# Optimization experiments

Hardware: AMD Instinct MI355X
Metric: run time of the kernel (lower is better)

The kernel has to match this reference:

```python
import jax, jax.numpy as jnp
import numpy as np

N_ATOM = 10000
D = 256
N_EDGE = 160000
BN_EPS = 1e-6


def _bn_eval(x, g, b, m, v):
    # BatchNorm1d in eval mode
    return (x - m) * jax.lax.rsqrt(v + BN_EPS) * g + b


def setup_inputs() -> dict:
    key = jax.random.key(0)
    ks = jax.random.split(key, 12)
    def glorot(k, shape):
        fan_in = shape[-1]
        return jax.random.normal(k, shape, dtype=jnp.float32) / np.sqrt(fan_in)
    inp = {
        'atom': jax.random.normal(ks[0], (N_ATOM, D), dtype=jnp.float32),
        'bond_index': jax.random.randint(ks[1], (2, N_EDGE), 0, N_ATOM, dtype=jnp.int32),
        # align: Linear(2D -> 1) + BN(1)
        'W_align': glorot(ks[2], (1, 2 * D)),
        'b_align': jnp.zeros((1,), jnp.float32),
        'bn_a_g': jnp.ones((1,), jnp.float32),
        'bn_a_b': jnp.zeros((1,), jnp.float32),
        'bn_a_m': jnp.zeros((1,), jnp.float32),
        'bn_a_v': jnp.ones((1,), jnp.float32),
        # attend: Linear(D -> D) + BN(D)
        'W_att': glorot(ks[3], (D, D)),
        'b_att': jnp.zeros((D,), jnp.float32),
        'bn_t_g': jnp.ones((D,), jnp.float32),
        'bn_t_b': jnp.zeros((D,), jnp.float32),
        'bn_t_m': jnp.zeros((D,), jnp.float32),
        'bn_t_v': jnp.ones((D,), jnp.float32),
        # GRUCell(D, D): weights stacked [r; z; n] as in torch
        'W_ih': glorot(ks[4], (3 * D, D)),
        'W_hh': glorot(ks[5], (3 * D, D)),
        'b_ih': jnp.zeros((3 * D,), jnp.float32),
        'b_hh': jnp.zeros((3 * D,), jnp.float32),
    }
    return inp


def reference(atom, bond_index, W_align, b_align, bn_a_g, bn_a_b, bn_a_m, bn_a_v,
              W_att, b_att, bn_t_g, bn_t_b, bn_t_m, bn_t_v,
              W_ih, W_hh, b_ih, b_hh):
    num_atom = atom.shape[0]
    src = bond_index[0]
    dst = bond_index[1]

    # gather + concat: [E, 2D]
    feat_align = jnp.concatenate([atom[src], atom[dst]], axis=-1)
    # align score: Linear(2D->1) + BN + leaky_relu -> [E, 1]
    s = feat_align @ W_align.T + b_align
    s = _bn_eval(s, bn_a_g, bn_a_b, bn_a_m, bn_a_v)
    s = jax.nn.leaky_relu(s, negative_slope=0.01)

    # segment softmax over edges grouped by src atom
    seg_max = jax.ops.segment_max(s, src, num_segments=num_atom)  # [N, 1]
    e = jnp.exp(s - seg_max[src])
    denom = jax.ops.segment_sum(e, src, num_segments=num_atom)    # [N, 1]
    attn = e / (denom[src] + 1e-8)                                # [E, 1]

    # attend: Linear(D->D) + BN on gathered dst features
    h = atom[dst] @ W_att.T + b_att
    h = _bn_eval(h, bn_t_g, bn_t_b, bn_t_m, bn_t_v)

    # weighted scatter-add aggregation -> [N, D], then ELU
    context = jax.ops.segment_sum(attn * h, src, num_segments=num_atom)
    context = jax.nn.elu(context)

    # GRUCell: input=context, hidden=atom
    gi = context @ W_ih.T + b_ih   # [N, 3D]
    gh = atom @ W_hh.T + b_hh      # [N, 3D]
    i_r, i_z, i_n = jnp.split(gi, 3, axis=-1)
    h_r, h_z, h_n = jnp.split(gh, 3, axis=-1)
    r = jax.nn.sigmoid(i_r + h_r)
    z = jax.nn.sigmoid(i_z + h_z)
    n = jnp.tanh(i_n + r * h_n)
    update = (1.0 - z) * n + z * atom
    return update
```

## Files before the change

kernel.cpp:

```cpp
#include <hip/hip_runtime.h>
#include <hip/hip_bf16.h>

#define D 256

typedef __attribute__((ext_vector_type(8))) short bf16x8;
typedef __attribute__((ext_vector_type(4))) short s16x4;
typedef __attribute__((ext_vector_type(4))) float f32x4;

#define MFMA __builtin_amdgcn_mfma_f32_16x16x32_bf16

__device__ __forceinline__ float s2f(short u) {
    union { unsigned int i; float f; } c;
    c.i = ((unsigned int)(unsigned short)u) << 16;
    return c.f;
}
__device__ __forceinline__ short f2s(float f) {
    union { float f; unsigned int u; } c; c.f = f;
    unsigned int u = c.u;
    u += 0x7fffu + ((u >> 16) & 1u);
    return (short)(u >> 16);
}

__global__ __launch_bounds__(256) void prep_kernel(
    const float* __restrict__ atom, short* __restrict__ atom_bf,
    const float* __restrict__ W_align, const float* __restrict__ b_align,
    const float* __restrict__ g, const float* __restrict__ bb,
    const float* __restrict__ mn, const float* __restrict__ vr,
    float* __restrict__ p0p, float* __restrict__ p1p,
    const float* __restrict__ Wa, short* __restrict__ Wa_bf,
    const float* __restrict__ Wi, short* __restrict__ Wi_bf,
    const float* __restrict__ Wh, short* __restrict__ Wh_bf,
    int* __restrict__ cnt, int* __restrict__ cursor,
    int N, int NROWB, int WCVTB)
{
    int b = blockIdx.x, tid = threadIdx.x;
    if (b < NROWB) {
        int wave = tid >> 6, lane = tid & 63;
        int row = b * 4 + wave;
        if (row >= N) return;
        float4 a = *(const float4*)(atom + (size_t)row * D + lane * 4);
        s16x4 o; o[0] = f2s(a.x); o[1] = f2s(a.y); o[2] = f2s(a.z); o[3] = f2s(a.w);
        ((s16x4*)(atom_bf + (size_t)row * D))[lane] = o;
        float4 w0 = *(const float4*)(W_align + lane * 4);
        float4 w1 = *(const float4*)(W_align + D + lane * 4);
        float d0 = a.x * w0.x + a.y * w0.y + a.z * w0.z + a.w * w0.w;
        float d1 = a.x * w1.x + a.y * w1.y + a.z * w1.z + a.w * w1.w;
        #pragma unroll
        for (int s = 32; s > 0; s >>= 1) {
            d0 += __shfl_xor(d0, s, 64);
            d1 += __shfl_xor(d1, s, 64);
        }
        if (lane == 0) {
            float A = rsqrtf(vr[0] + 1e-6f) * g[0];
            p0p[row] = A * (d0 + b_align[0]) + bb[0] - A * mn[0];
            p1p[row] = A * d1;
        }
        return;
    }
    b -= NROWB;
    if (b < WCVTB) {
        int nW4 = D * D / 4, nG4 = 3 * D * D / 4;
        int j = b * 256 + tid;
        const float* src; short* dst;
        if (j < nW4) { src = Wa; dst = Wa_bf; }
        else { j -= nW4;
            if (j < nG4) { src = Wi; dst = Wi_bf; }
            else { j -= nG4;
                if (j < nG4) { src = Wh; dst = Wh_bf; }
                else return;
            }
        }
        float4 v = ((const float4*)src)[j];
        s16x4 o; o[0] = f2s(v.x); o[1] = f2s(v.y); o[2] = f2s(v.z); o[3] = f2s(v.w);
        ((s16x4*)dst)[j] = o;
        return;
    }
    b -= WCVTB;
    int i = b * 256 + tid;
    if (i < N) { cnt[i] = 0; cursor[i] = 0; }
}

__global__ __launch_bounds__(256) void count_kernel(const int* __restrict__ src, int* cnt, int E) {
    int e = blockIdx.x * 256 + threadIdx.x;
    if (e < E) atomicAdd(&cnt[src[e]], 1);
}

__global__ __launch_bounds__(1024) void scan_kernel(const int* __restrict__ cnt, int* __restrict__ off, int N) {
    __shared__ int sums[1024];
    int t = threadIdx.x;
    int CH = (N + 1023) / 1024;
    int beg = t * CH;
    int end = beg + CH; if (end > N) end = N;
    int s = 0;
    for (int i = beg; i < end; i++) s += cnt[i];
    sums[t] = s;
    __syncthreads();
    for (int d = 1; d < 1024; d <<= 1) {
        int x = (t >= d) ? sums[t - d] : 0;
        __syncthreads();
        sums[t] += x;
        __syncthreads();
    }
    int run = (t > 0) ? sums[t - 1] : 0;
    for (int i = beg; i < end; i++) { off[i] = run; run += cnt[i]; }
    if (end == N) off[N] = run;
}

__global__ __launch_bounds__(256) void fill_kernel(const int* __restrict__ src, const int* __restrict__ dst,
                                                   const int* __restrict__ off, int* cursor, int* dlist, int E) {
    int e = blockIdx.x * 256 + threadIdx.x;
    if (e < E) {
        int s = src[e];
        int p = atomicAdd(&cursor[s], 1);
        dlist[off[s] + p] = dst[e];
    }
}

__global__ __launch_bounds__(256) void hA_kernel(
    const short* __restrict__ atom_bf, const short* __restrict__ W_bf,
    const float* __restrict__ bias,
    const float* __restrict__ g, const float* __restrict__ bb,
    const float* __restrict__ mn, const float* __restrict__ vr,
    short* __restrict__ hA, int N, int NB)
{
    __shared__ short Bs[2048 * 8];
    int bi = blockIdx.x;
    int xcd = bi & 7, rest = bi >> 3;
    int cb = rest & 3, gh = rest >> 2;
    int gg = gh * 8 + xcd;
    if (gg >= NB) return;
    int c0 = cb * 64;
    int tid = threadIdx.x;
    for (int c = tid; c < 2048; c += 256) {
        int l15c = c & 15, quadc = (c >> 4) & 3, t2 = c >> 6;
        int kkc = t2 & 7, jc = t2 >> 3;
        bf16x8 v = *(const bf16x8*)(W_bf + (size_t)(c0 + jc * 16 + l15c) * D + quadc * 8 + kkc * 32);
        *(bf16x8*)(&Bs[c * 8]) = v;
    }
    __syncthreads();

    int wave = tid >> 6, lane = tid & 63;
    int quad = lane >> 4, l15 = lane & 15;
    int m0 = gg * 128 + wave * 16;
    int ar0 = m0 + l15;       if (ar0 > N - 1) ar0 = N - 1;
    int ar1 = m0 + 64 + l15;  if (ar1 > N - 1) ar1 = N - 1;
    const short* ap0 = atom_bf + (size_t)ar0 * D + quad * 8;
    const short* ap1 = atom_bf + (size_t)ar1 * D + quad * 8;
    const short* lb = &Bs[lane * 8];
    f32x4 acc[2][4];
    #pragma unroll
    for (int t = 0; t < 2; t++)
        #pragma unroll
        for (int j = 0; j < 4; j++) acc[t][j] = (f32x4){0,0,0,0};
    #pragma unroll
    for (int kk = 0; kk < 8; kk++) {
        int k = kk * 32;
        bf16x8 a0 = *(const bf16x8*)(ap0 + k);
        bf16x8 a1 = *(const bf16x8*)(ap1 + k);
        bf16x8 b0 = *(const bf16x8*)(lb + (0 * 8 + kk) * 512);
        bf16x8 b1 = *(const bf16x8*)(lb + (1 * 8 + kk) * 512);
        bf16x8 b2 = *(const bf16x8*)(lb + (2 * 8 + kk) * 512);
        bf16x8 b3 = *(const bf16x8*)(lb + (3 * 8 + kk) * 512);
        acc[0][0] = MFMA(a0, b0, acc[0][0], 0, 0, 0);
        acc[0][1] = MFMA(a0, b1, acc[0][1], 0, 0, 0);
        acc[0][2] = MFMA(a0, b2, acc[0][2], 0, 0, 0);
        acc[0][3] = MFMA(a0, b3, acc[0][3], 0, 0, 0);
        acc[1][0] = MFMA(a1, b0, acc[1][0], 0, 0, 0);
        acc[1][1] = MFMA(a1, b1, acc[1][1], 0, 0, 0);
        acc[1][2] = MFMA(a1, b2, acc[1][2], 0, 0, 0);
        acc[1][3] = MFMA(a1, b3, acc[1][3], 0, 0, 0);
    }
    #pragma unroll
    for (int j = 0; j < 4; j++) {
        int col = c0 + j * 16 + l15;
        float sc = rsqrtf(vr[col] + 1e-6f) * g[col];
        float sh = bb[col] - mn[col] * sc;
        float bi_ = bias[col];
        #pragma unroll
        for (int t = 0; t < 2; t++) {
            #pragma unroll
            for (int r = 0; r < 4; r++) {
                int row = m0 + t * 64 + quad * 4 + r;
                if (row < N) hA[(size_t)row * D + col] = f2s((acc[t][j][r] + bi_) * sc + sh);
            }
        }
    }
}

__global__ __launch_bounds__(256) void agg_kernel(
    const int* __restrict__ off, const int* __restrict__ dlist,
    const float* __restrict__ p0p, const float* __restrict__ p1p,
    const short* __restrict__ hA, short* __restrict__ ctx, int N)
{
    int w = (blockIdx.x * blockDim.x + threadIdx.x) >> 6;
    int lane = threadIdx.x & 63;
    if (w >= N) return;
    int beg = off[w], end = off[w + 1];
    float u = p0p[w];
    int half = lane >> 5, l32 = lane & 31;
    float acc[8] = {0.f,0.f,0.f,0.f,0.f,0.f,0.f,0.f};
    float se = 0.f;
    for (int j = beg + half; j < end; j += 2) {
        int d = dlist[j];
        float x = u + p1p[d];
        x = x > 0.f ? x : 0.01f * x;
        float e = __expf(x);
        se += e;
        bf16x8 h = *(const bf16x8*)(hA + (size_t)d * D + l32 * 8);
        #pragma unroll
        for (int i = 0; i < 8; i++) acc[i] += e * s2f(h[i]);
    }
    se += __shfl_xor(se, 32, 64);
    #pragma unroll
    for (int i = 0; i < 8; i++) acc[i] += __shfl_xor(acc[i], 32, 64);
    if (half == 0) {
        float inv = 1.f / (se + 1e-8f);
        bf16x8 o;
        #pragma unroll
        for (int i = 0; i < 8; i++) {
            float v = acc[i] * inv;
            v = v > 0.f ? v : __expf(v) - 1.f;
            o[i] = f2s(v);
        }
        *(bf16x8*)(ctx + (size_t)w * D + l32 * 8) = o;
    }
}

__global__ __launch_bounds__(256) void gru_kernel(
    const short* __restrict__ ctx, const short* __restrict__ atom_bf,
    const short* __restrict__ W_ih, const short* __restrict__ W_hh,
    const float* __restrict__ b_ih, const float* __restrict__ b_hh,
    float* __restrict__ out, int N, int NB)
{
    __shared__ short Bs[3072 * 8];
    int bi = blockIdx.x;
    int xcd = bi & 7, rest = bi >> 3;
    int cb = rest & 15, gh = rest >> 4;
    int gg = gh * 8 + xcd;
    if (gg >= NB) return;
    int c0 = cb * 16;
    int tid = threadIdx.x;
    for (int c = tid; c < 3072; c += 256) {
        int l15c = c & 15, quadc = (c >> 4) & 3, t2 = c >> 6;
        int kkc = t2 & 7, gate = t2 >> 3;
        const short* srcp = (gate < 3)
            ? W_ih + (size_t)(gate * 256 + c0 + l15c) * D + quadc * 8 + kkc * 32
            : W_hh + (size_t)((gate - 3) * 256 + c0 + l15c) * D + quadc * 8 + kkc * 32;
        *(bf16x8*)(&Bs[c * 8]) = *(const bf16x8*)srcp;
    }
    __syncthreads();

    int wave = tid >> 6, lane = tid & 63;
    int quad = lane >> 4, l15 = lane & 15;
    int m0 = gg * 128 + wave * 16;
    int ar0 = m0 + l15;       if (ar0 > N - 1) ar0 = N - 1;
    int ar1 = m0 + 64 + l15;  if (ar1 > N - 1) ar1 = N - 1;
    const short* cp0 = ctx + (size_t)ar0 * D + quad * 8;
    const short* ap0 = atom_bf + (size_t)ar0 * D + quad * 8;
    const short* cp1 = ctx + (size_t)ar1 * D + quad * 8;
    const short* ap1 = atom_bf + (size_t)ar1 * D + quad * 8;
    const short* lb = &Bs[lane * 8];
    f32x4 gi[2][3], gh_[2][3];
    #pragma unroll
    for (int t = 0; t < 2; t++)
        #pragma unroll
        for (int j = 0; j < 3; j++) { gi[t][j] = (f32x4){0,0,0,0}; gh_[t][j] = (f32x4){0,0,0,0}; }
    #pragma unroll
    for (int kk = 0; kk < 8; kk++) {
        int k = kk * 32;
        bf16x8 c0v = *(const bf16x8*)(cp0 + k);
        bf16x8 a0v = *(const bf16x8*)(ap0 + k);
        bf16x8 c1v = *(const bf16x8*)(cp1 + k);
        bf16x8 a1v = *(const bf16x8*)(ap1 + k);
        bf16x8 bir = *(const bf16x8*)(lb + (0 * 8 + kk) * 512);
        bf16x8 biz = *(const bf16x8*)(lb + (1 * 8 + kk) * 512);
        bf16x8 bin = *(const bf16x8*)(lb + (2 * 8 + kk) * 512);
        bf16x8 bhr = *(const bf16x8*)(lb + (3 * 8 + kk) * 512);
        bf16x8 bhz = *(const bf16x8*)(lb + (4 * 8 + kk) * 512);
        bf16x8 bhn = *(const bf16x8*)(lb + (5 * 8 + kk) * 512);
        gi[0][0] = MFMA(c0v, bir, gi[0][0], 0, 0, 0);
        gi[0][1] = MFMA(c0v, biz, gi[0][1], 0, 0, 0);
        gi[0][2] = MFMA(c0v, bin, gi[0][2], 0, 0, 0);
        gh_[0][0] = MFMA(a0v, bhr, gh_[0][0], 0, 0, 0);
        gh_[0][1] = MFMA(a0v, bhz, gh_[0][1], 0, 0, 0);
        gh_[0][2] = MFMA(a0v, bhn, gh_[0][2], 0, 0, 0);
        gi[1][0] = MFMA(c1v, bir, gi[1][0], 0, 0, 0);
        gi[1][1] = MFMA(c1v, biz, gi[1][1], 0, 0, 0);
        gi[1][2] = MFMA(c1v, bin, gi[1][2], 0, 0, 0);
        gh_[1][0] = MFMA(a1v, bhr, gh_[1][0], 0, 0, 0);
        gh_[1][1] = MFMA(a1v, bhz, gh_[1][1], 0, 0, 0);
        gh_[1][2] = MFMA(a1v, bhn, gh_[1][2], 0, 0, 0);
    }
    int col = c0 + l15;
    float bir_s = b_ih[col], biz_s = b_ih[col + 256], bin_s = b_ih[col + 512];
    float bhr_s = b_hh[col], bhz_s = b_hh[col + 256], bhn_s = b_hh[col + 512];
    #pragma unroll
    for (int t = 0; t < 2; t++) {
        #pragma unroll
        for (int r = 0; r < 4; r++) {
            int row = m0 + t * 64 + quad * 4 + r;
            if (row < N) {
                float rr = 1.f / (1.f + __expf(-(gi[t][0][r] + bir_s + gh_[t][0][r] + bhr_s)));
                float zz = 1.f / (1.f + __expf(-(gi[t][1][r] + biz_s + gh_[t][1][r] + bhz_s)));
                float nn = tanhf(gi[t][2][r] + bin_s + rr * (gh_[t][2][r] + bhn_s));
                float at = s2f(atom_bf[(size_t)row * D + col]);
                out[(size_t)row * D + col] = (1.f - zz) * nn + zz * at;
            }
        }
    }
}

extern "C" void kernel_launch(void* const* d_in, const int* in_sizes, int n_in,
                              void* d_out, int out_size, void* d_ws, size_t ws_size,
                              hipStream_t stream) {
    const float* atom    = (const float*)d_in[0];
    const int*   bond    = (const int*)d_in[1];
    const float* W_align = (const float*)d_in[2];
    const float* b_align = (const float*)d_in[3];
    const float* bn_a_g  = (const float*)d_in[4];
    const float* bn_a_b  = (const float*)d_in[5];
    const float* bn_a_m  = (const float*)d_in[6];
    const float* bn_a_v  = (const float*)d_in[7];
    const float* W_att   = (const float*)d_in[8];
    const float* b_att   = (const float*)d_in[9];
    const float* bn_t_g  = (const float*)d_in[10];
    const float* bn_t_b  = (const float*)d_in[11];
    const float* bn_t_m  = (const float*)d_in[12];
    const float* bn_t_v  = (const float*)d_in[13];
    const float* W_ih    = (const float*)d_in[14];
    const float* W_hh    = (const float*)d_in[15];
    const float* b_ih    = (const float*)d_in[16];
    const float* b_hh    = (const float*)d_in[17];

    int N = in_sizes[0] / D;
    int E = in_sizes[1] / 2;
    const int* src = bond;
    const int* dst = bond + E;

    char* w = (char*)d_ws;
    size_t o = 0;
    auto alloc = [&](size_t bytes) {
        void* p = w + o;
        o = (o + bytes + 255) & ~(size_t)255;
        return p;
    };
    int*   cnt     = (int*)alloc((size_t)N * 4);
    int*   cursor  = (int*)alloc((size_t)N * 4);
    int*   offv    = (int*)alloc((size_t)(N + 1) * 4);
    int*   dlist   = (int*)alloc((size_t)E * 4);
    float* p0p     = (float*)alloc((size_t)N * 4);
    float* p1p     = (float*)alloc((size_t)N * 4);
    short* hA      = (short*)alloc((size_t)N * D * 2);
    short* ctx     = (short*)alloc((size_t)N * D * 2);
    short* atom_bf = (short*)alloc((size_t)N * D * 2);
    short* Watt_bf = (short*)alloc((size_t)D * D * 2);
    short* Wih_bf  = (short*)alloc((size_t)3 * D * D * 2);
    short* Whh_bf  = (short*)alloc((size_t)3 * D * D * 2);

    int NROWB = (N + 3) / 4;
    int nWtot4 = (D * D + 2 * 3 * D * D) / 4;
    int WCVTB = (nWtot4 + 255) / 256;
    int INITB = (N + 255) / 256;
    prep_kernel<<<NROWB + WCVTB + INITB, 256, 0, stream>>>(
        atom, atom_bf, W_align, b_align, bn_a_g, bn_a_b, bn_a_m, bn_a_v, p0p, p1p,
        W_att, Watt_bf, W_ih, Wih_bf, W_hh, Whh_bf, cnt, cursor, N, NROWB, WCVTB);
    count_kernel<<<(E + 255) / 256, 256, 0, stream>>>(src, cnt, E);
    scan_kernel<<<1, 1024, 0, stream>>>(cnt, offv, N);
    fill_kernel<<<(E + 255) / 256, 256, 0, stream>>>(src, dst, offv, cursor, dlist, E);

    int NB = (N + 127) / 128;
    int GH = (NB + 7) / 8;
    hA_kernel<<<8 * 4 * GH, 256, 0, stream>>>(
        atom_bf, Watt_bf, b_att, bn_t_g, bn_t_b, bn_t_m, bn_t_v, hA, N, NB);
    agg_kernel<<<((size_t)N * 64 + 255) / 256, 256, 0, stream>>>(
        offv, dlist, p0p, p1p, hA, ctx, N);
    gru_kernel<<<8 * 16 * GH, 256, 0, stream>>>(
        ctx, atom_bf, Wih_bf, Whh_bf, b_ih, b_hh, (float*)d_out, N, NB);
}
```

Baseline: 192.9 us.

## Merge prep, CSR build, scan and attend GEMM into one cooperative kernel

Replaces five separate launches (prep, count, single-block scan, fill, hA GEMM) with one cooperative persistent kernel that uses grid.sync between phases. The serial single-block 1024-thread scan becomes a two-level parallel block scan, and the hA tiles are processed in a grid-stride loop. This removes launch gaps and the slow scan, but adds grid-wide barriers, caps the grid at 512 blocks, and loses the XCD-aware tile mapping of the old hA kernel.

Result: slower. 337.7 us (+75.1%).

```diff
diff --git a/kernel.cpp b/kernel.cpp
--- a/kernel.cpp
+++ b/kernel.cpp
@@ -1,7 +1,10 @@
 #include <hip/hip_runtime.h>
 #include <hip/hip_bf16.h>
+#include <hip/hip_cooperative_groups.h>
 
 #define D 256
+
+namespace cg = cooperative_groups;
 
 typedef __attribute__((ext_vector_type(8))) short bf16x8;
 typedef __attribute__((ext_vector_type(4))) short s16x4;
@@ -21,167 +24,178 @@
     return (short)(u >> 16);
 }
 
-__global__ __launch_bounds__(256) void prep_kernel(
-    const float* __restrict__ atom, short* __restrict__ atom_bf,
-    const float* __restrict__ W_align, const float* __restrict__ b_align,
-    const float* __restrict__ g, const float* __restrict__ bb,
-    const float* __restrict__ mn, const float* __restrict__ vr,
-    float* __restrict__ p0p, float* __restrict__ p1p,
-    const float* __restrict__ Wa, short* __restrict__ Wa_bf,
-    const float* __restrict__ Wi, short* __restrict__ Wi_bf,
-    const float* __restrict__ Wh, short* __restrict__ Wh_bf,
-    int* __restrict__ cnt, int* __restrict__ cursor,
-    int N, int NROWB, int WCVTB)
+struct FrontArgs {
+    const float* atom; short* atom_bf;
+    const float* W_align; const float* b_align;
+    const float* g_a; const float* b_a; const float* m_a; const float* v_a;
+    float* p0p; float* p1p;
+    const float* Wa; short* Wa_bf;
+    const float* Wi; short* Wi_bf;
+    const float* Wh; short* Wh_bf;
+    const int* src; const int* dst;
+    int* cnt; int* cursor; int* off; int* dlist; int* blocksum;
+    const float* bias_att; const float* g_t; const float* b_t;
+    const float* m_t; const float* v_t;
+    short* hA;
+    int N; int E; int NB;
+};
+
+__global__ __launch_bounds__(256) void front_kernel(FrontArgs P)
 {
-    int b = blockIdx.x, tid = threadIdx.x;
-    if (b < NROWB) {
-        int wave = tid >> 6, lane = tid & 63;
-        int row = b * 4 + wave;
-        if (row >= N) return;
-        float4 a = *(const float4*)(atom + (size_t)row * D + lane * 4);
-        s16x4 o; o[0] = f2s(a.x); o[1] = f2s(a.y); o[2] = f2s(a.z); o[3] = f2s(a.w);
-        ((s16x4*)(atom_bf + (size_t)row * D))[lane] = o;
-        float4 w0 = *(const float4*)(W_align + lane * 4);
-        float4 w1 = *(const float4*)(W_align + D + lane * 4);
-        float d0 = a.x * w0.x + a.y * w0.y + a.z * w0.z + a.w * w0.w;
-        float d1 = a.x * w1.x + a.y * w1.y + a.z * w1.z + a.w * w1.w;
-        #pragma unroll
-        for (int s = 32; s > 0; s >>= 1) {
-            d0 += __shfl_xor(d0, s, 64);
-            d1 += __shfl_xor(d1, s, 64);
-        }
-        if (lane == 0) {
-            float A = rsqrtf(vr[0] + 1e-6f) * g[0];
-            p0p[row] = A * (d0 + b_align[0]) + bb[0] - A * mn[0];
-            p1p[row] = A * d1;
-        }
-        return;
-    }
-    b -= NROWB;
-    if (b < WCVTB) {
+    cg::grid_group grid = cg::this_grid();
+    __shared__ short Bs[2048 * 8];
+    int* sI = (int*)Bs;
+    const int nblk = gridDim.x;
+    const int tid = threadIdx.x;
+    const int wave = tid >> 6, lane = tid & 63;
+
+    {
+        int NROWB = (P.N + 3) / 4;
+        for (int b = blockIdx.x; b < NROWB; b += nblk) {
+            int row = b * 4 + wave;
+            if (row < P.N) {
+                float4 a = *(const float4*)(P.atom + (size_t)row * D + lane * 4);
+                s16x4 o; o[0] = f2s(a.x); o[1] = f2s(a.y); o[2] = f2s(a.z); o[3] = f2s(a.w);
+                ((s16x4*)(P.atom_bf + (size_t)row * D))[lane] = o;
+                float4 w0 = *(const float4*)(P.W_align + lane * 4);
+                float4 w1 = *(const float4*)(P.W_align + D + lane * 4);
+                float d0 = a.x * w0.x + a.y * w0.y + a.z * w0.z + a.w * w0.w;
+                float d1 = a.x * w1.x + a.y * w1.y + a.z * w1.z + a.w * w1.w;
+                #pragma unroll
+                for (int s = 32; s > 0; s >>= 1) {
+                    d0 += __shfl_xor(d0, s, 64);
+                    d1 += __shfl_xor(d1, s, 64);
+                }
+                if (lane == 0) {
+                    float A = rsqrtf(P.v_a[0] + 1e-6f) * P.g_a[0];
+                    P.p0p[row] = A * (d0 + P.b_align[0]) + P.b_a[0] - A * P.m_a[0];
+                    P.p1p[row] = A * d1;
+                }
+            }
+        }
         int nW4 = D * D / 4, nG4 = 3 * D * D / 4;
-        int j = b * 256 + tid;
-        const float* src; short* dst;
-        if (j < nW4) { src = Wa; dst = Wa_bf; }
-        else { j -= nW4;
-            if (j < nG4) { src = Wi; dst = Wi_bf; }
-            else { j -= nG4;
-                if (j < nG4) { src = Wh; dst = Wh_bf; }
-                else return;
+        int nTot = nW4 + 2 * nG4;
+        for (int j0 = blockIdx.x * 256 + tid; j0 < nTot; j0 += nblk * 256) {
+            int j = j0; const float* srcp; short* dstp;
+            if (j < nW4) { srcp = P.Wa; dstp = P.Wa_bf; }
+            else { j -= nW4;
+                if (j < nG4) { srcp = P.Wi; dstp = P.Wi_bf; }
+                else { j -= nG4; srcp = P.Wh; dstp = P.Wh_bf; }
             }
-        }
-        float4 v = ((const float4*)src)[j];
-        s16x4 o; o[0] = f2s(v.x); o[1] = f2s(v.y); o[2] = f2s(v.z); o[3] = f2s(v.w);
-        ((s16x4*)dst)[j] = o;
-        return;
-    }
-    b -= WCVTB;
-    int i = b * 256 + tid;
-    if (i < N) { cnt[i] = 0; cursor[i] = 0; }
-}
-
-__global__ __launch_bounds__(256) void count_kernel(const int* __restrict__ src, int* cnt, int E) {
-    int e = blockIdx.x * 256 + threadIdx.x;
-    if (e < E) atomicAdd(&cnt[src[e]], 1);
-}
-
-__global__ __launch_bounds__(1024) void scan_kernel(const int* __restrict__ cnt, int* __restrict__ off, int N) {
-    __shared__ int sums[1024];
-    int t = threadIdx.x;
-    int CH = (N + 1023) / 1024;
-    int beg = t * CH;
-    int end = beg + CH; if (end > N) end = N;
-    int s = 0;
-    for (int i = beg; i < end; i++) s += cnt[i];
-    sums[t] = s;
-    __syncthreads();
-    for (int d = 1; d < 1024; d <<= 1) {
-        int x = (t >= d) ? sums[t - d] : 0;
-        __syncthreads();
-        sums[t] += x;
-        __syncthreads();
-    }
-    int run = (t > 0) ? sums[t - 1] : 0;
-    for (int i = beg; i < end; i++) { off[i] = run; run += cnt[i]; }
-    if (end == N) off[N] = run;
-}
-
-__global__ __launch_bounds__(256) void fill_kernel(const int* __restrict__ src, const int* __restrict__ dst,
-                                                   const int* __restrict__ off, int* cursor, int* dlist, int E) {
-    int e = blockIdx.x * 256 + threadIdx.x;
-    if (e < E) {
-        int s = src[e];
-        int p = atomicAdd(&cursor[s], 1);
-        dlist[off[s] + p] = dst[e];
-    }
-}
-
-__global__ __launch_bounds__(256) void hA_kernel(
-    const short* __restrict__ atom_bf, const short* __restrict__ W_bf,
-    const float* __restrict__ bias,
-    const float* __restrict__ g, const float* __restrict__ bb,
-    const float* __restrict__ mn, const float* __restrict__ vr,
-    short* __restrict__ hA, int N, int NB)
-{
-    __shared__ short Bs[2048 * 8];
-    int bi = blockIdx.x;
-    int xcd = bi & 7, rest = bi >> 3;
-    int cb = rest & 3, gh = rest >> 2;
-    int gg = gh * 8 + xcd;
-    if (gg >= NB) return;
-    int c0 = cb * 64;
-    int tid = threadIdx.x;
-    for (int c = tid; c < 2048; c += 256) {
-        int l15c = c & 15, quadc = (c >> 4) & 3, t2 = c >> 6;
-        int kkc = t2 & 7, jc = t2 >> 3;
-        bf16x8 v = *(const bf16x8*)(W_bf + (size_t)(c0 + jc * 16 + l15c) * D + quadc * 8 + kkc * 32);
-        *(bf16x8*)(&Bs[c * 8]) = v;
-    }
-    __syncthreads();
-
-    int wave = tid >> 6, lane = tid & 63;
-    int quad = lane >> 4, l15 = lane & 15;
-    int m0 = gg * 128 + wave * 16;
-    int ar0 = m0 + l15;       if (ar0 > N - 1) ar0 = N - 1;
-    int ar1 = m0 + 64 + l15;  if (ar1 > N - 1) ar1 = N - 1;
-    const short* ap0 = atom_bf + (size_t)ar0 * D + quad * 8;
-    const short* ap1 = atom_bf + (size_t)ar1 * D + quad * 8;
-    const short* lb = &Bs[lane * 8];
-    f32x4 acc[2][4];
-    #pragma unroll
-    for (int t = 0; t < 2; t++)
-        #pragma unroll
-        for (int j = 0; j < 4; j++) acc[t][j] = (f32x4){0,0,0,0};
-    #pragma unroll
-    for (int kk = 0; kk < 8; kk++) {
-        int k = kk * 32;
-        bf16x8 a0 = *(const bf16x8*)(ap0 + k);
-        bf16x8 a1 = *(const bf16x8*)(ap1 + k);
-        bf16x8 b0 = *(const bf16x8*)(lb + (0 * 8 + kk) * 512);
-        bf16x8 b1 = *(const bf16x8*)(lb + (1 * 8 + kk) * 512);
-        bf16x8 b2 = *(const bf16x8*)(lb + (2 * 8 + kk) * 512);
-        bf16x8 b3 = *(const bf16x8*)(lb + (3 * 8 + kk) * 512);
-        acc[0][0] = MFMA(a0, b0, acc[0][0], 0, 0, 0);
-        acc[0][1] = MFMA(a0, b1, acc[0][1], 0, 0, 0);
-        acc[0][2] = MFMA(a0, b2, acc[0][2], 0, 0, 0);
-        acc[0][3] = MFMA(a0, b3, acc[0][3], 0, 0, 0);
-        acc[1][0] = MFMA(a1, b0, acc[1][0], 0, 0, 0);
-        acc[1][1] = MFMA(a1, b1, acc[1][1], 0, 0, 0);
-        acc[1][2] = MFMA(a1, b2, acc[1][2], 0, 0, 0);
-        acc[1][3] = MFMA(a1, b3, acc[1][3], 0, 0, 0);
-    }
-    #pragma unroll
-    for (int j = 0; j < 4; j++) {
-        int col = c0 + j * 16 + l15;
-        float sc = rsqrtf(vr[col] + 1e-6f) * g[col];
-        float sh = bb[col] - mn[col] * sc;
-        float bi_ = bias[col];
-        #pragma unroll
-        for (int t = 0; t < 2; t++) {
+            float4 v = ((const float4*)srcp)[j];
+            s16x4 o; o[0] = f2s(v.x); o[1] = f2s(v.y); o[2] = f2s(v.z); o[3] = f2s(v.w);
+            ((s16x4*)dstp)[j] = o;
+        }
+        for (int i = blockIdx.x * 256 + tid; i < P.N; i += nblk * 256) {
+            P.cnt[i] = 0; P.cursor[i] = 0;
+        }
+    }
+    grid.sync();
+
+    for (int e = blockIdx.x * 256 + tid; e < P.E; e += nblk * 256)
+        atomicAdd(&P.cnt[P.src[e]], 1);
+    grid.sync();
+
+    int NCH = (P.N + 255) / 256;
+    for (int b = blockIdx.x; b < NCH; b += nblk) {
+        int i = b * 256 + tid;
+        int v = (i < P.N) ? P.cnt[i] : 0;
+        int s = v;
+        #pragma unroll
+        for (int sh = 1; sh < 64; sh <<= 1) s += __shfl_xor(s, sh, 64);
+        if (lane == 0) sI[wave] = s;
+        __syncthreads();
+        if (tid == 0) P.blocksum[b] = sI[0] + sI[1] + sI[2] + sI[3];
+        __syncthreads();
+    }
+    grid.sync();
+
+    for (int b = blockIdx.x; b < NCH; b += nblk) {
+        for (int k2 = tid; k2 < NCH; k2 += 256) sI[64 + k2] = P.blocksum[k2];
+        __syncthreads();
+        int base = 0;
+        for (int k = 0; k < b; k++) base += sI[64 + k];
+        int i = b * 256 + tid;
+        int v = (i < P.N) ? P.cnt[i] : 0;
+        int inc = v;
+        #pragma unroll
+        for (int sh = 1; sh < 64; sh <<= 1) {
+            int t = __shfl_up(inc, (unsigned)sh, 64);
+            if (lane >= sh) inc += t;
+        }
+        if (lane == 63) sI[wave] = inc;
+        __syncthreads();
+        int wbase = 0;
+        for (int k = 0; k < wave; k++) wbase += sI[k];
+        int excl = base + wbase + inc - v;
+        if (i < P.N) P.off[i] = excl;
+        if (i == P.N - 1) P.off[P.N] = excl + v;
+        __syncthreads();
+    }
+    grid.sync();
+
+    for (int e = blockIdx.x * 256 + tid; e < P.E; e += nblk * 256) {
+        int s = P.src[e];
+        int p = atomicAdd(&P.cursor[s], 1);
+        P.dlist[P.off[s] + p] = P.dst[e];
+    }
+
+    int NTILE = P.NB * 4;
+    for (int t = blockIdx.x; t < NTILE; t += nblk) {
+        __syncthreads();
+        int gg = t >> 2, cb = t & 3;
+        int c0 = cb * 64;
+        for (int c = tid; c < 2048; c += 256) {
+            int l15c = c & 15, quadc = (c >> 4) & 3, t2 = c >> 6;
+            int kkc = t2 & 7, jc = t2 >> 3;
+            bf16x8 v = *(const bf16x8*)(P.Wa_bf + (size_t)(c0 + jc * 16 + l15c) * D + quadc * 8 + kkc * 32);
+            *(bf16x8*)(&Bs[c * 8]) = v;
+        }
+        __syncthreads();
+
+        int quad = lane >> 4, l15 = lane & 15;
+        int m0 = gg * 128 + wave * 16;
+        int ar0 = m0 + l15;       if (ar0 > P.N - 1) ar0 = P.N - 1;
+        int ar1 = m0 + 64 + l15;  if (ar1 > P.N - 1) ar1 = P.N - 1;
+        const short* ap0 = P.atom_bf + (size_t)ar0 * D + quad * 8;
+        const short* ap1 = P.atom_bf + (size_t)ar1 * D + quad * 8;
+        const short* lb = &Bs[lane * 8];
+        f32x4 acc[2][4];
+        #pragma unroll
+        for (int tt = 0; tt < 2; tt++)
             #pragma unroll
-            for (int r = 0; r < 4; r++) {
-                int row = m0 + t * 64 + quad * 4 + r;
-                if (row < N) hA[(size_t)row * D + col] = f2s((acc[t][j][r] + bi_) * sc + sh);
+            for (int j = 0; j < 4; j++) acc[tt][j] = (f32x4){0,0,0,0};
+        #pragma unroll
+        for (int kk = 0; kk < 8; kk++) {
+            int k = kk * 32;
+            bf16x8 a0 = *(const bf16x8*)(ap0 + k);
+            bf16x8 a1 = *(const bf16x8*)(ap1 + k);
+            bf16x8 b0 = *(const bf16x8*)(lb + (0 * 8 + kk) * 512);
+            bf16x8 b1 = *(const bf16x8*)(lb + (1 * 8 + kk) * 512);
+            bf16x8 b2 = *(const bf16x8*)(lb + (2 * 8 + kk) * 512);
+            bf16x8 b3 = *(const bf16x8*)(lb + (3 * 8 + kk) * 512);
+            acc[0][0] = MFMA(a0, b0, acc[0][0], 0, 0, 0);
+            acc[0][1] = MFMA(a0, b1, acc[0][1], 0, 0, 0);
+            acc[0][2] = MFMA(a0, b2, acc[0][2], 0, 0, 0);
+            acc[0][3] = MFMA(a0, b3, acc[0][3], 0, 0, 0);
+            acc[1][0] = MFMA(a1, b0, acc[1][0], 0, 0, 0);
+            acc[1][1] = MFMA(a1, b1, acc[1][1], 0, 0, 0);
+            acc[1][2] = MFMA(a1, b2, acc[1][2], 0, 0, 0);
+            acc[1][3] = MFMA(a1, b3, acc[1][3], 0, 0, 0);
+        }
+        #pragma unroll
+        for (int j = 0; j < 4; j++) {
+            int col = c0 + j * 16 + l15;
+            float sc = rsqrtf(P.v_t[col] + 1e-6f) * P.g_t[col];
+            float sh = P.b_t[col] - P.m_t[col] * sc;
+            float bi_ = P.bias_att[col];
+            #pragma unroll
+            for (int tt = 0; tt < 2; tt++) {
+                #pragma unroll
+                for (int r = 0; r < 4; r++) {
+                    int row = m0 + tt * 64 + quad * 4 + r;
+                    if (row < P.N) P.hA[(size_t)row * D + col] = f2s((acc[tt][j][r] + bi_) * sc + sh);
+                }
             }
         }
     }
@@ -344,36 +358,59 @@
         o = (o + bytes + 255) & ~(size_t)255;
         return p;
     };
-    int*   cnt     = (int*)alloc((size_t)N * 4);
-    int*   cursor  = (int*)alloc((size_t)N * 4);
-    int*   offv    = (int*)alloc((size_t)(N + 1) * 4);
-    int*   dlist   = (int*)alloc((size_t)E * 4);
-    float* p0p     = (float*)alloc((size_t)N * 4);
-    float* p1p     = (float*)alloc((size_t)N * 4);
-    short* hA      = (short*)alloc((size_t)N * D * 2);
-    short* ctx     = (short*)alloc((size_t)N * D * 2);
-    short* atom_bf = (short*)alloc((size_t)N * D * 2);
-    short* Watt_bf = (short*)alloc((size_t)D * D * 2);
-    short* Wih_bf  = (short*)alloc((size_t)3 * D * D * 2);
-    short* Whh_bf  = (short*)alloc((size_t)3 * D * D * 2);
-
-    int NROWB = (N + 3) / 4;
-    int nWtot4 = (D * D + 2 * 3 * D * D) / 4;
-    int WCVTB = (nWtot4 + 255) / 256;
-    int INITB = (N + 255) / 256;
-    prep_kernel<<<NROWB + WCVTB + INITB, 256, 0, stream>>>(
-        atom, atom_bf, W_align, b_align, bn_a_g, bn_a_b, bn_a_m, bn_a_v, p0p, p1p,
-        W_att, Watt_bf, W_ih, Wih_bf, W_hh, Whh_bf, cnt, cursor, N, NROWB, WCVTB);
-    count_kernel<<<(E + 255) / 256, 256, 0, stream>>>(src, cnt, E);
-    scan_kernel<<<1, 1024, 0, stream>>>(cnt, offv, N);
-    fill_kernel<<<(E + 255) / 256, 256, 0, stream>>>(src, dst, offv, cursor, dlist, E);
+    int*   cnt      = (int*)alloc((size_t)N * 4);
+    int*   cursor   = (int*)alloc((size_t)N * 4);
+    int*   offv     = (int*)alloc((size_t)(N + 1) * 4);
+    int*   dlist    = (int*)alloc((size_t)E * 4);
+    int*   blocksum = (int*)alloc((size_t)((N + 255) / 256 + 1) * 4);
+    float* p0p      = (float*)alloc((size_t)N * 4);
+    float* p1p      = (float*)alloc((size_t)N * 4);
+    short* hA       = (short*)alloc((size_t)N * D * 2);
+    short* ctx      = (short*)alloc((size_t)N * D * 2);
+    short* atom_bf  = (short*)alloc((size_t)N * D * 2);
+    short* Watt_bf  = (short*)alloc((size_t)D * D * 2);
+    short* Wih_bf   = (short*)alloc((size_t)3 * D * D * 2);
+    short* Whh_bf   = (short*)alloc((size_t)3 * D * D * 2);
 
     int NB = (N + 127) / 128;
-    int GH = (NB + 7) / 8;
-    hA_kernel<<<8 * 4 * GH, 256, 0, stream>>>(
-        atom_bf, Watt_bf, b_att, bn_t_g, bn_t_b, bn_t_m, bn_t_v, hA, N, NB);
+
+    static int s_grid = 0;
+    if (s_grid == 0) {
+        int nb = 0;
+        hipError_t err = hipOccupancyMaxActiveBlocksPerMultiprocessor(
+            &nb, (const void*)front_kernel, 256, 0);
+        int dev = 0; hipGetDevice(&dev);
+        int smcount = 0;
+        hipDeviceGetAttribute(&smcount, hipDeviceAttributeMultiprocessorCount, dev);
+        if (err != hipSuccess || nb < 1) nb = 1;
+        if (smcount <= 0) smcount = 256;
+        long cap = (long)nb * (long)smcount;
+        s_grid = (int)(cap < 512 ? cap : 512);
+        if (s_grid < 1) s_grid = 256;
+    }
+
+    FrontArgs P;
+    P.atom = atom; P.atom_bf = atom_bf;
+    P.W_align = W_align; P.b_align = b_align;
+    P.g_a = bn_a_g; P.b_a = bn_a_b; P.m_a = bn_a_m; P.v_a = bn_a_v;
+    P.p0p = p0p; P.p1p = p1p;
+    P.Wa = W_att; P.Wa_bf = Watt_bf;
+    P.Wi = W_ih; P.Wi_bf = Wih_bf;
+    P.Wh = W_hh; P.Wh_bf = Whh_bf;
+    P.src = src; P.dst = dst;
+    P.cnt = cnt; P.cursor = cursor; P.off = offv; P.dlist = dlist; P.blocksum = blocksum;
+    P.bias_att = b_att; P.g_t = bn_t_g; P.b_t = bn_t_b; P.m_t = bn_t_m; P.v_t = bn_t_v;
+    P.hA = hA;
+    P.N = N; P.E = E; P.NB = NB;
+
+    void* args[] = { (void*)&P };
+    hipLaunchCooperativeKernel((const void*)front_kernel, dim3(s_grid), dim3(256),
+                               args, 0, stream);
+
     agg_kernel<<<((size_t)N * 64 + 255) / 256, 256, 0, stream>>>(
         offv, dlist, p0p, p1p, hA, ctx, N);
+
+    int GH = (NB + 7) / 8;
     gru_kernel<<<8 * 16 * GH, 256, 0, stream>>>(
         ctx, atom_bf, Wih_bf, Whh_bf, b_ih, b_hh, (float*)d_out, N, NB);
 }
```

## Merge CSR build stages into prep and hA kernels, widen agg edge parallelism

Applied to the files above, without the earlier changes.

Counting edges now happens inside the prep kernel, and the offset scan runs in one extra block of the attend GEMM kernel. The scan uses wave shuffles and seeds a per-row cursor, so fill writes directly at the cursor position. This cuts the launch count from seven to six, at the cost of a separate small zero kernel. The aggregation kernel now processes four edges at once per wave, with 16 lanes per edge each reading 16 columns, instead of two. That raises memory-level parallelism but adds more shuffle reductions.

After: 196.2 us. No clear change (+1.7%).

```diff
diff --git a/kernel.cpp b/kernel.cpp
--- a/kernel.cpp
+++ b/kernel.cpp
@@ -19,6 +19,11 @@
     unsigned int u = c.u;
     u += 0x7fffu + ((u >> 16) & 1u);
     return (short)(u >> 16);
+}
+
+__global__ __launch_bounds__(256) void zero_kernel(int* __restrict__ cnt, int N) {
+    int i = blockIdx.x * 256 + threadIdx.x;
+    if (i < N) cnt[i] = 0;
 }
 
 __global__ __launch_bounds__(256) void prep_kernel(
@@ -30,8 +35,8 @@
     const float* __restrict__ Wa, short* __restrict__ Wa_bf,
     const float* __restrict__ Wi, short* __restrict__ Wi_bf,
     const float* __restrict__ Wh, short* __restrict__ Wh_bf,
-    int* __restrict__ cnt, int* __restrict__ cursor,
-    int N, int NROWB, int WCVTB)
+    const int* __restrict__ src, int* __restrict__ cnt,
+    int N, int E, int NROWB, int WCVTB)
 {
     int b = blockIdx.x, tid = threadIdx.x;
     if (b < NROWB) {
@@ -61,62 +66,27 @@
     if (b < WCVTB) {
         int nW4 = D * D / 4, nG4 = 3 * D * D / 4;
         int j = b * 256 + tid;
-        const float* src; short* dst;
-        if (j < nW4) { src = Wa; dst = Wa_bf; }
+        const float* srcp; short* dstp;
+        if (j < nW4) { srcp = Wa; dstp = Wa_bf; }
         else { j -= nW4;
-            if (j < nG4) { src = Wi; dst = Wi_bf; }
+            if (j < nG4) { srcp = Wi; dstp = Wi_bf; }
             else { j -= nG4;
-                if (j < nG4) { src = Wh; dst = Wh_bf; }
+                if (j < nG4) { srcp = Wh; dstp = Wh_bf; }
                 else return;
             }
         }
-        float4 v = ((const float4*)src)[j];
+        float4 v = ((const float4*)srcp)[j];
         s16x4 o; o[0] = f2s(v.x); o[1] = f2s(v.y); o[2] = f2s(v.z); o[3] = f2s(v.w);
-        ((s16x4*)dst)[j] = o;
+        ((s16x4*)dstp)[j] = o;
         return;
     }
     b -= WCVTB;
-    int i = b * 256 + tid;
-    if (i < N) { cnt[i] = 0; cursor[i] = 0; }
-}
-
-__global__ __launch_bounds__(256) void count_kernel(const int* __restrict__ src, int* cnt, int E) {
-    int e = blockIdx.x * 256 + threadIdx.x;
+    int e = b * 256 + tid;
     if (e < E) atomicAdd(&cnt[src[e]], 1);
 }
 
-__global__ __launch_bounds__(1024) void scan_kernel(const int* __restrict__ cnt, int* __restrict__ off, int N) {
-    __shared__ int sums[1024];
-    int t = threadIdx.x;
-    int CH = (N + 1023) / 1024;
-    int beg = t * CH;
-    int end = beg + CH; if (end > N) end = N;
-    int s = 0;
-    for (int i = beg; i < end; i++) s += cnt[i];
-    sums[t] = s;
-    __syncthreads();
-    for (int d = 1; d < 1024; d <<= 1) {
-        int x = (t >= d) ? sums[t - d] : 0;
-        __syncthreads();
-        sums[t] += x;
-        __syncthreads();
-    }
-    int run = (t > 0) ? sums[t - 1] : 0;
-    for (int i = beg; i < end; i++) { off[i] = run; run += cnt[i]; }
-    if (end == N) off[N] = run;
-}
-
-__global__ __launch_bounds__(256) void fill_kernel(const int* __restrict__ src, const int* __restrict__ dst,
-                                                   const int* __restrict__ off, int* cursor, int* dlist, int E) {
-    int e = blockIdx.x * 256 + threadIdx.x;
-    if (e < E) {
-        int s = src[e];
-        int p = atomicAdd(&cursor[s], 1);
-        dlist[off[s] + p] = dst[e];
-    }
-}
-
-__global__ __launch_bounds__(256) void hA_kernel(
+__global__ __launch_bounds__(256) void scan_hA_kernel(
+    const int* __restrict__ cnt, int* __restrict__ off, int* __restrict__ cur,
     const short* __restrict__ atom_bf, const short* __restrict__ W_bf,
     const float* __restrict__ bias,
     const float* __restrict__ g, const float* __restrict__ bb,
@@ -124,13 +94,38 @@
     short* __restrict__ hA, int N, int NB)
 {
     __shared__ short Bs[2048 * 8];
-    int bi = blockIdx.x;
+    int tid = threadIdx.x;
+    if (blockIdx.x == 0) {
+        int* sI = (int*)Bs;
+        int CH = (N + 255) / 256;
+        int beg = tid * CH;
+        int end = beg + CH; if (end > N) end = N;
+        int s = 0;
+        for (int i = beg; i < end; i++) s += cnt[i];
+        int lane = tid & 63, wv = tid >> 6;
+        int inc = s;
+        #pragma unroll
+        for (int sh = 1; sh < 64; sh <<= 1) {
+            int t = __shfl_up(inc, (unsigned)sh, 64);
+            if (lane >= sh) inc += t;
+        }
+        if (lane == 63) sI[wv] = inc;
+        __syncthreads();
+        int wbase = 0;
+        for (int k = 0; k < wv; k++) wbase += sI[k];
+        int run = wbase + inc - s;
+        for (int i = beg; i < end; i++) {
+            off[i] = run; cur[i] = run; run += cnt[i];
+        }
+        if (tid == 255) off[N] = run;
+        return;
+    }
+    int bi = blockIdx.x - 1;
     int xcd = bi & 7, rest = bi >> 3;
     int cb = rest & 3, gh = rest >> 2;
     int gg = gh * 8 + xcd;
     if (gg >= NB) return;
     int c0 = cb * 64;
-    int tid = threadIdx.x;
     for (int c = tid; c < 2048; c += 256) {
         int l15c = c & 15, quadc = (c >> 4) & 3, t2 = c >> 6;
         int kkc = t2 & 7, jc = t2 >> 3;
@@ -187,6 +182,16 @@
     }
 }
 
+__global__ __launch_bounds__(256) void fill_kernel(const int* __restrict__ src, const int* __restrict__ dst,
+                                                   int* cur, int* dlist, int E) {
+    int e = blockIdx.x * 256 + threadIdx.x;
+    if (e < E) {
+        int s = src[e];
+        int p = atomicAdd(&cur[s], 1);
+        dlist[p] = dst[e];
+    }
+}
+
 __global__ __launch_bounds__(256) void agg_kernel(
     const int* __restrict__ off, const int* __restrict__ dlist,
     const float* __restrict__ p0p, const float* __restrict__ p1p,
@@ -197,32 +202,47 @@
     if (w >= N) return;
     int beg = off[w], end = off[w + 1];
     float u = p0p[w];
-    int half = lane >> 5, l32 = lane & 31;
-    float acc[8] = {0.f,0.f,0.f,0.f,0.f,0.f,0.f,0.f};
+    int grp = lane >> 4, l16 = lane & 15;
+    float acc[16];
+    #pragma unroll
+    for (int i = 0; i < 16; i++) acc[i] = 0.f;
     float se = 0.f;
-    for (int j = beg + half; j < end; j += 2) {
+    for (int j = beg + grp; j < end; j += 4) {
         int d = dlist[j];
         float x = u + p1p[d];
         x = x > 0.f ? x : 0.01f * x;
         float e = __expf(x);
         se += e;
-        bf16x8 h = *(const bf16x8*)(hA + (size_t)d * D + l32 * 8);
-        #pragma unroll
-        for (int i = 0; i < 8; i++) acc[i] += e * s2f(h[i]);
-    }
+        const short* hp = hA + (size_t)d * D + l16 * 16;
+        bf16x8 h0 = *(const bf16x8*)(hp);
+        bf16x8 h1 = *(const bf16x8*)(hp + 8);
+        #pragma unroll
+        for (int i = 0; i < 8; i++) acc[i]     += e * s2f(h0[i]);
+        #pragma unroll
+        for (int i = 0; i < 8; i++) acc[8 + i] += e * s2f(h1[i]);
+    }
+    se += __shfl_xor(se, 16, 64);
     se += __shfl_xor(se, 32, 64);
     #pragma unroll
-    for (int i = 0; i < 8; i++) acc[i] += __shfl_xor(acc[i], 32, 64);
-    if (half == 0) {
+    for (int i = 0; i < 16; i++) {
+        acc[i] += __shfl_xor(acc[i], 16, 64);
+        acc[i] += __shfl_xor(acc[i], 32, 64);
+    }
+    if (grp == 0) {
         float inv = 1.f / (se + 1e-8f);
-        bf16x8 o;
+        bf16x8 o0, o1;
         #pragma unroll
         for (int i = 0; i < 8; i++) {
-            float v = acc[i] * inv;
-            v = v > 0.f ? v : __expf(v) - 1.f;
-            o[i] = f2s(v);
-        }
-        *(bf16x8*)(ctx + (size_t)w * D + l32 * 8) = o;
+            float v0 = acc[i] * inv;
+            v0 = v0 > 0.f ? v0 : __expf(v0) - 1.f;
+            o0[i] = f2s(v0);
+            float v1 = acc[8 + i] * inv;
+            v1 = v1 > 0.f ? v1 : __expf(v1) - 1.f;
+            o1[i] = f2s(v1);
+        }
+        short* cp = ctx + (size_t)w * D + l16 * 16;
+        *(bf16x8*)cp = o0;
+        *(bf16x8*)(cp + 8) = o1;
     }
 }
 
@@ -345,7 +365,7 @@
         return p;
     };
     int*   cnt     = (int*)alloc((size_t)N * 4);
-    int*   cursor  = (int*)alloc((size_t)N * 4);
+    int*   cur     = (int*)alloc((size_t)N * 4);
     int*   offv    = (int*)alloc((size_t)(N + 1) * 4);
     int*   dlist   = (int*)alloc((size_t)E * 4);
     float* p0p     = (float*)alloc((size_t)N * 4);
@@ -360,18 +380,17 @@
     int NROWB = (N + 3) / 4;
     int nWtot4 = (D * D + 2 * 3 * D * D) / 4;
     int WCVTB = (nWtot4 + 255) / 256;
-    int INITB = (N + 255) / 256;
-    prep_kernel<<<NROWB + WCVTB + INITB, 256, 0, stream>>>(
-        atom, atom_bf, W_align, b_align, bn_a_g, bn_a_b, bn_a_m, bn_a_v, p0p, p1p,
-        W_att, Watt_bf, W_ih, Wih_bf, W_hh, Whh_bf, cnt, cursor, N, NROWB, WCVTB);
-    count_kernel<<<(E + 255) / 256, 256, 0, stream>>>(src, cnt, E);
-    scan_kernel<<<1, 1024, 0, stream>>>(cnt, offv, N);
-    fill_kernel<<<(E + 255) / 256, 256, 0, stream>>>(src, dst, offv, cursor, dlist, E);
-
+    int EB = (E + 255) / 256;
     int NB = (N + 127) / 128;
     int GH = (NB + 7) / 8;
-    hA_kernel<<<8 * 4 * GH, 256, 0, stream>>>(
-        atom_bf, Watt_bf, b_att, bn_t_g, bn_t_b, bn_t_m, bn_t_v, hA, N, NB);
+
+    zero_kernel<<<(N + 255) / 256, 256, 0, stream>>>(cnt, N);
+    prep_kernel<<<NROWB + WCVTB + EB, 256, 0, stream>>>(
+        atom, atom_bf, W_align, b_align, bn_a_g, bn_a_b, bn_a_m, bn_a_v, p0p, p1p,
+        W_att, Watt_bf, W_ih, Wih_bf, W_hh, Whh_bf, src, cnt, N, E, NROWB, WCVTB);
+    scan_hA_kernel<<<1 + 8 * 4 * GH, 256, 0, stream>>>(
+        cnt, offv, cur, atom_bf, Watt_bf, b_att, bn_t_g, bn_t_b, bn_t_m, bn_t_v, hA, N, NB);
+    fill_kernel<<<EB, 256, 0, stream>>>(src, dst, cur, dlist, E);
     agg_kernel<<<((size_t)N * 64 + 255) / 256, 256, 0, stream>>>(
         offv, dlist, p0p, p1p, hA, ctx, N);
     gru_kernel<<<8 * 16 * GH, 256, 0, stream>>>(
```
